# Optimization experiments

Hardware: AMD Instinct MI355X
Metric: run time of the kernel (lower is better)

## Reference

```python
import jax, jax.numpy as jnp
import numpy as np

N = 50000
F_IN = 128
HID0, HID1 = 64, 32
HEADS = 2
E = 800000
NEG_SLOPE = 0.2


def gat_conv(x, edge_index, W, att_src, att_dst, bias, heads, out_ch, concat):
    """PyG-style GATConv (add_self_loops=True, negative_slope=0.2, eval mode)."""
    n = x.shape[0]
    loop = jnp.arange(n, dtype=edge_index.dtype)
    src = jnp.concatenate([edge_index[0], loop])  # message sources (x_j)
    dst = jnp.concatenate([edge_index[1], loop])  # message targets (x_i)
    h = (x @ W).reshape(n, heads, out_ch)                # [N,H,C]
    a_src = jnp.einsum('nhc,hc->nh', h, att_src)          # [N,H]
    a_dst = jnp.einsum('nhc,hc->nh', h, att_dst)          # [N,H]
    e = jax.nn.leaky_relu(a_src[src] + a_dst[dst], NEG_SLOPE)  # [E+N,H]
    # segment softmax over incoming edges of each destination node
    m = jax.ops.segment_max(e, dst, num_segments=n)
    m = jnp.where(jnp.isfinite(m), m, 0.0)
    p = jnp.exp(e - m[dst])
    s = jax.ops.segment_sum(p, dst, num_segments=n)
    alpha = p / (s[dst] + 1e-16)                          # [E+N,H]
    msg = h[src] * alpha[:, :, None]                      # [E+N,H,C]
    out = jax.ops.segment_sum(msg, dst, num_segments=n)   # [N,H,C]
    out = out.reshape(n, heads * out_ch) if concat else out.mean(axis=1)
    return out + bias


def setup_inputs() -> dict:
    key = jax.random.key(0)
    ks = jax.random.split(key, 10)
    sc1 = 1.0 / np.sqrt(F_IN)
    sc2 = 1.0 / np.sqrt(HEADS * HID0)
    return {
        'x': jax.random.normal(ks[0], (N, F_IN), dtype=jnp.float32),
        'edge_index': jax.random.randint(ks[1], (2, E), 0, N, dtype=jnp.int64),
        'W1': jax.random.normal(ks[2], (F_IN, HEADS * HID0), dtype=jnp.float32) * sc1,
        'att_src1': jax.random.normal(ks[3], (HEADS, HID0), dtype=jnp.float32) * sc1,
        'att_dst1': jax.random.normal(ks[4], (HEADS, HID0), dtype=jnp.float32) * sc1,
        'bias1': jnp.zeros((HEADS * HID0,), dtype=jnp.float32),
        'W2': jax.random.normal(ks[5], (HEADS * HID0, HEADS * HID1), dtype=jnp.float32) * sc2,
        'att_src2': jax.random.normal(ks[6], (HEADS, HID1), dtype=jnp.float32) * sc2,
        'att_dst2': jax.random.normal(ks[7], (HEADS, HID1), dtype=jnp.float32) * sc2,
        'bias2': jnp.zeros((HID1,), dtype=jnp.float32),
    }


def reference(x, edge_index, W1, att_src1, att_dst1, bias1, W2, att_src2, att_dst2, bias2):
    h = gat_conv(x, edge_index, W1, att_src1, att_dst1, bias1, HEADS, HID0, concat=True)
    h = jax.nn.relu(h)  # Dropout(0.6) is identity in eval mode
    out = gat_conv(h, edge_index, W2, att_src2, att_dst2, bias2, HEADS, HID1, concat=False)
    return out
```

## Files before the change

### kernel.cpp

```cpp
#include <hip/hip_runtime.h>
#include <hip/hip_bf16.h>

#define NN 50000
#define FIN 128
#define NH 2
#define C1 64
#define C2 32
#define NE 800000
#define NEG 0.2f

typedef unsigned int uint32;

__device__ __forceinline__ float lrelu(float v) { return v > 0.0f ? v : NEG * v; }
__device__ __forceinline__ float dot4(float4 a, float4 b) {
    return a.x * b.x + a.y * b.y + a.z * b.z + a.w * b.w;
}
__device__ __forceinline__ uint32 packbf2(float a, float b) {
    uint32 ua = __float_as_uint(a), ub = __float_as_uint(b);
    ua += 0x7fffu + ((ua >> 16) & 1u);
    ub += 0x7fffu + ((ub >> 16) & 1u);
    return (ua >> 16) | (ub & 0xffff0000u);
}

__global__ void zero_ints(int* __restrict__ a, int n) {
    for (int i = blockIdx.x * blockDim.x + threadIdx.x; i < n;
         i += gridDim.x * blockDim.x) a[i] = 0;
}

__global__ void hist_dst(const int* __restrict__ ei, int* __restrict__ deg) {
    const int i = blockIdx.x * blockDim.x + threadIdx.x;
    if (i >= NE) return;
    atomicAdd(&deg[ei[NE + i]], 1);
}

__global__ void scan_blocks(const int* __restrict__ deg, int* __restrict__ offs,
                            int* __restrict__ bsum) {
    __shared__ int sm[256];
    const int t = threadIdx.x;
    const int i = blockIdx.x * 256 + t;
    const int v = (i < NN) ? deg[i] : 0;
    sm[t] = v;
    __syncthreads();
    int x = v;
    #pragma unroll
    for (int d = 1; d < 256; d <<= 1) {
        const int y = (t >= d) ? sm[t - d] : 0;
        __syncthreads();
        x += y; sm[t] = x;
        __syncthreads();
    }
    if (i < NN) offs[i] = x - v;
    if (t == 255) bsum[blockIdx.x] = x;
}

__global__ void scan_bsums(int* __restrict__ bsum, int nb) {
    __shared__ int sm[256];
    const int t = threadIdx.x;
    const int v = (t < nb) ? bsum[t] : 0;
    sm[t] = v;
    __syncthreads();
    int x = v;
    #pragma unroll
    for (int d = 1; d < 256; d <<= 1) {
        const int y = (t >= d) ? sm[t - d] : 0;
        __syncthreads();
        x += y; sm[t] = x;
        __syncthreads();
    }
    if (t < nb) bsum[t] = x - v;
}

__global__ void scan_add(int* __restrict__ offs, const int* __restrict__ bsum) {
    const int i = blockIdx.x * 256 + threadIdx.x;
    if (i < NN) offs[i] += bsum[blockIdx.x];
}

__global__ void csr_scatter(const int* __restrict__ ei, const int* __restrict__ offs,
                            int* __restrict__ fill, int* __restrict__ esrc) {
    const int i = blockIdx.x * blockDim.x + threadIdx.x;
    if (i >= NE) return;
    const int src = ei[i], dst = ei[NE + i];
    const int pos = offs[dst] + atomicAdd(&fill[dst], 1);
    esrc[pos] = src;
}

template<int BN, bool RELU_BIAS, bool WRITE_Y, bool WRITE_H16>
__global__ __launch_bounds__(256, 2) void gemm_k128(const float* __restrict__ X,
                                                    const float* __restrict__ Wm,
                                                    const float* __restrict__ bias,
                                                    const float* __restrict__ attS,
                                                    const float* __restrict__ attD,
                                                    float* __restrict__ Y,
                                                    uint32* __restrict__ H16,
                                                    float* __restrict__ asrcO,
                                                    float* __restrict__ adstO, int M) {
    constexpr int GROUPS = BN / 16;
    constexpr int BM = 256 / GROUPS;
    constexpr int CS = BN / 4;
    __shared__ __align__(16) float Xs[BM][33];
    __shared__ __align__(16) float Ws[32][BN];

    const int tid = threadIdx.x;
    const int r  = tid / GROUPS;
    const int g  = tid % GROUPS;
    const int rowBase = blockIdx.x * BM;

    float4 acc0 = {0,0,0,0}, acc1 = {0,0,0,0}, acc2 = {0,0,0,0}, acc3 = {0,0,0,0};

    for (int kk = 0; kk < 4; ++kk) {
        constexpr int XV = BM * 8;
        #pragma unroll
        for (int i = tid; i < XV; i += 256) {
            const int xr = i >> 3, xc = (i & 7) * 4;
            const int grow = rowBase + xr;
            float4 v = {0,0,0,0};
            if (grow < M) {
                v = *reinterpret_cast<const float4*>(&X[grow * FIN + kk * 32 + xc]);
                if (RELU_BIAS) {
                    const float4 b = *reinterpret_cast<const float4*>(&bias[kk * 32 + xc]);
                    v.x = fmaxf(v.x + b.x, 0.0f);
                    v.y = fmaxf(v.y + b.y, 0.0f);
                    v.z = fmaxf(v.z + b.z, 0.0f);
                    v.w = fmaxf(v.w + b.w, 0.0f);
                }
            }
            Xs[xr][xc] = v.x; Xs[xr][xc+1] = v.y; Xs[xr][xc+2] = v.z; Xs[xr][xc+3] = v.w;
        }
        constexpr int WV = 32 * BN / 4;
        #pragma unroll
        for (int i = tid; i < WV; i += 256) {
            const int wr = i / (BN / 4), wc = (i % (BN / 4)) * 4;
            *reinterpret_cast<float4*>(&Ws[wr][wc]) =
                *reinterpret_cast<const float4*>(&Wm[(kk * 32 + wr) * BN + wc]);
        }
        __syncthreads();
        #pragma unroll
        for (int k = 0; k < 32; ++k) {
            const float xv = Xs[r][k];
            const float4 w0 = *reinterpret_cast<const float4*>(&Ws[k][g * 4]);
            const float4 w1 = *reinterpret_cast<const float4*>(&Ws[k][g * 4 + CS]);
            const float4 w2 = *reinterpret_cast<const float4*>(&Ws[k][g * 4 + 2 * CS]);
            const float4 w3 = *reinterpret_cast<const float4*>(&Ws[k][g * 4 + 3 * CS]);
            acc0.x += xv * w0.x; acc0.y += xv * w0.y; acc0.z += xv * w0.z; acc0.w += xv * w0.w;
            acc1.x += xv * w1.x; acc1.y += xv * w1.y; acc1.z += xv * w1.z; acc1.w += xv * w1.w;
            acc2.x += xv * w2.x; acc2.y += xv * w2.y; acc2.z += xv * w2.z; acc2.w += xv * w2.w;
            acc3.x += xv * w3.x; acc3.y += xv * w3.y; acc3.z += xv * w3.z; acc3.w += xv * w3.w;
        }
        __syncthreads();
    }

    const int grow = rowBase + r;
    if (grow < M) {
        if (WRITE_Y) {
            float* yrow = &Y[grow * BN + g * 4];
            *reinterpret_cast<float4*>(yrow)          = acc0;
            *reinterpret_cast<float4*>(yrow + CS)     = acc1;
            *reinterpret_cast<float4*>(yrow + 2 * CS) = acc2;
            *reinterpret_cast<float4*>(yrow + 3 * CS) = acc3;
        }
        if (WRITE_H16) {
            uint32* hrow = &H16[grow * (BN / 2)];
            uint2 u;
            u.x = packbf2(acc0.x, acc0.y); u.y = packbf2(acc0.z, acc0.w);
            *reinterpret_cast<uint2*>(&hrow[g * 2])              = u;
            u.x = packbf2(acc1.x, acc1.y); u.y = packbf2(acc1.z, acc1.w);
            *reinterpret_cast<uint2*>(&hrow[g * 2 + CS / 2])     = u;
            u.x = packbf2(acc2.x, acc2.y); u.y = packbf2(acc2.z, acc2.w);
            *reinterpret_cast<uint2*>(&hrow[g * 2 + CS])         = u;
            u.x = packbf2(acc3.x, acc3.y); u.y = packbf2(acc3.z, acc3.w);
            *reinterpret_cast<uint2*>(&hrow[g * 2 + 3 * CS / 2]) = u;
        }
    }
    const float4* avs = reinterpret_cast<const float4*>(attS);
    const float4* avd = reinterpret_cast<const float4*>(attD);
    float ps0 = dot4(acc0, avs[g])              + dot4(acc1, avs[g + GROUPS]);
    float ps1 = dot4(acc2, avs[g + 2 * GROUPS]) + dot4(acc3, avs[g + 3 * GROUPS]);
    float pd0 = dot4(acc0, avd[g])              + dot4(acc1, avd[g + GROUPS]);
    float pd1 = dot4(acc2, avd[g + 2 * GROUPS]) + dot4(acc3, avd[g + 3 * GROUPS]);
    #pragma unroll
    for (int d = 1; d < GROUPS; d <<= 1) {
        ps0 += __shfl_xor(ps0, d);
        ps1 += __shfl_xor(ps1, d);
        pd0 += __shfl_xor(pd0, d);
        pd1 += __shfl_xor(pd1, d);
    }
    if (g == 0 && grow < M) {
        asrcO[grow * 2]     = ps0;
        asrcO[grow * 2 + 1] = ps1;
        adstO[grow * 2]     = pd0;
        adstO[grow * 2 + 1] = pd1;
    }
}

__global__ __launch_bounds__(256) void gat_dst1(const int* __restrict__ esrc,
                                                const int* __restrict__ offs,
                                                const uint32* __restrict__ H16,
                                                const float* __restrict__ asrc,
                                                const float* __restrict__ adst,
                                                float* __restrict__ out) {
    const int wid  = (blockIdx.x * blockDim.x + threadIdx.x) >> 6;
    const int lane = threadIdx.x & 63;
    if (wid >= NN) return;
    const int dst = wid;
    const int beg = offs[dst];
    const int end = (dst == NN - 1) ? NE : offs[dst + 1];
    const int deg = end - beg;
    const float2 ad = *reinterpret_cast<const float2*>(&adst[dst * 2]);

    int   s0  = 0;
    float pe0 = -INFINITY, pe1 = -INFINITY;
    float m0  = -INFINITY, m1  = -INFINITY;
    for (int j = lane; j < deg; j += 64) {
        const int s = esrc[beg + j];
        const float2 a = *reinterpret_cast<const float2*>(&asrc[s * 2]);
        const float f0 = lrelu(a.x + ad.x);
        const float f1 = lrelu(a.y + ad.y);
        if (j == lane) { s0 = s; pe0 = f0; pe1 = f1; }
        m0 = fmaxf(m0, f0); m1 = fmaxf(m1, f1);
    }
    const float2 aself = *reinterpret_cast<const float2*>(&asrc[dst * 2]);
    const float es0 = lrelu(aself.x + ad.x);
    const float es1 = lrelu(aself.y + ad.y);
    m0 = fmaxf(m0, es0); m1 = fmaxf(m1, es1);
    #pragma unroll
    for (int d = 1; d < 64; d <<= 1) {
        m0 = fmaxf(m0, __shfl_xor(m0, d));
        m1 = fmaxf(m1, __shfl_xor(m1, d));
    }
    const int h = lane >> 5;
    const float m = h ? m1 : m0;

    float l;
    float2 acc;
    {
        const float px = __expf((h ? es1 : es0) - m);
        l = px;
        const uint32 u = H16[dst * 64 + lane];
        acc.x = px * __uint_as_float(u << 16);
        acc.y = px * __uint_as_float(u & 0xffff0000u);
    }
    const int jmax = deg < 64 ? deg : 64;
    for (int j = 0; j < jmax; ++j) {
        const int s = __shfl(s0, j);
        const float t0 = __shfl(pe0, j), t1 = __shfl(pe1, j);
        const float p = __expf((h ? t1 : t0) - m);
        const uint32 u = H16[s * 64 + lane];
        l += p;
        acc.x += p * __uint_as_float(u << 16);
        acc.y += p * __uint_as_float(u & 0xffff0000u);
    }
    for (int j = 64; j < deg; ++j) {
        const int s = esrc[beg + j];
        const float2 a = *reinterpret_cast<const float2*>(&asrc[s * 2]);
        const float p = __expf(lrelu((h ? a.y : a.x) + (h ? ad.y : ad.x)) - m);
        const uint32 u = H16[s * 64 + lane];
        l += p;
        acc.x += p * __uint_as_float(u << 16);
        acc.y += p * __uint_as_float(u & 0xffff0000u);
    }
    const float inv = 1.0f / (l + 1e-16f);
    float2 res; res.x = acc.x * inv; res.y = acc.y * inv;
    *reinterpret_cast<float2*>(&out[dst * 128 + lane * 2]) = res;
}

__global__ __launch_bounds__(256) void gat_dst2(const int* __restrict__ esrc,
                                                const int* __restrict__ offs,
                                                const float* __restrict__ Hf,
                                                const float* __restrict__ asrc,
                                                const float* __restrict__ adst,
                                                const float* __restrict__ bias,
                                                float* __restrict__ out) {
    const int wid  = (blockIdx.x * blockDim.x + threadIdx.x) >> 6;
    const int lane = threadIdx.x & 63;
    if (wid >= NN) return;
    const int dst = wid;
    const int beg = offs[dst];
    const int end = (dst == NN - 1) ? NE : offs[dst + 1];
    const int deg = end - beg;
    const float2 ad = *reinterpret_cast<const float2*>(&adst[dst * 2]);

    int   s0  = 0;
    float pe0 = -INFINITY, pe1 = -INFINITY;
    float m0  = -INFINITY, m1  = -INFINITY;
    for (int j = lane; j < deg; j += 64) {
        const int s = esrc[beg + j];
        const float2 a = *reinterpret_cast<const float2*>(&asrc[s * 2]);
        const float f0 = lrelu(a.x + ad.x);
        const float f1 = lrelu(a.y + ad.y);
        if (j == lane) { s0 = s; pe0 = f0; pe1 = f1; }
        m0 = fmaxf(m0, f0); m1 = fmaxf(m1, f1);
    }
    const float2 aself = *reinterpret_cast<const float2*>(&asrc[dst * 2]);
    const float es0 = lrelu(aself.x + ad.x);
    const float es1 = lrelu(aself.y + ad.y);
    m0 = fmaxf(m0, es0); m1 = fmaxf(m1, es1);
    #pragma unroll
    for (int d = 1; d < 64; d <<= 1) {
        m0 = fmaxf(m0, __shfl_xor(m0, d));
        m1 = fmaxf(m1, __shfl_xor(m1, d));
    }
    const int h = lane >> 5;
    const float m = h ? m1 : m0;

    float l, acc;
    {
        const float px = __expf((h ? es1 : es0) - m);
        l = px;
        acc = px * Hf[dst * 64 + lane];
    }
    const int jmax = deg < 64 ? deg : 64;
    for (int j = 0; j < jmax; ++j) {
        const int s = __shfl(s0, j);
        const float t0 = __shfl(pe0, j), t1 = __shfl(pe1, j);
        const float p = __expf((h ? t1 : t0) - m);
        const float hv = Hf[s * 64 + lane];
        l += p;
        acc += p * hv;
    }
    for (int j = 64; j < deg; ++j) {
        const int s = esrc[beg + j];
        const float2 a = *reinterpret_cast<const float2*>(&asrc[s * 2]);
        const float p = __expf(lrelu((h ? a.y : a.x) + (h ? ad.y : ad.x)) - m);
        l += p;
        acc += p * Hf[s * 64 + lane];
    }
    float r = acc / (l + 1e-16f);
    r += __shfl_xor(r, 32);
    if (lane < 32) out[dst * 32 + lane] = 0.5f * r + bias[lane];
}

extern "C" void kernel_launch(void* const* d_in, const int* in_sizes, int n_in,
                              void* d_out, int out_size, void* d_ws, size_t ws_size,
                              hipStream_t stream) {
    const float* x   = (const float*)d_in[0];
    const int*   ei  = (const int*)d_in[1];
    const float* W1  = (const float*)d_in[2];
    const float* as1 = (const float*)d_in[3];
    const float* ad1 = (const float*)d_in[4];
    const float* b1  = (const float*)d_in[5];
    const float* W2  = (const float*)d_in[6];
    const float* as2 = (const float*)d_in[7];
    const float* ad2 = (const float*)d_in[8];
    const float* b2  = (const float*)d_in[9];
    float* out = (float*)d_out;

    float* ws = (float*)d_ws;
    size_t off = 0;
    float* out1  = ws + off; off += (size_t)NN * FIN;
    float* h2f   = ws + off; off += (size_t)NN * C1;
    float* asrc1 = ws + off; off += (size_t)NN * NH;
    float* adst1 = ws + off; off += (size_t)NN * NH;
    float* asrc2 = ws + off; off += (size_t)NN * NH;
    float* adst2 = ws + off; off += (size_t)NN * NH;
    uint32* h16  = (uint32*)(ws + off); off += (size_t)NN * 64;
    int* ibase = (int*)(ws + off);
    int* deg   = ibase;
    int* fill  = ibase + NN;
    int* offs  = ibase + 2 * NN;
    int* bsum  = ibase + 3 * NN;
    int* esrc  = ibase + 3 * NN + 256;

    const int B = 256;
    constexpr int NB_SCAN = (NN + 255) / 256;

    zero_ints<<<128, B, 0, stream>>>(deg, 2 * NN);
    hist_dst<<<(NE + B - 1) / B, B, 0, stream>>>(ei, deg);
    scan_blocks<<<NB_SCAN, 256, 0, stream>>>(deg, offs, bsum);
    scan_bsums<<<1, 256, 0, stream>>>(bsum, NB_SCAN);
    scan_add<<<NB_SCAN, 256, 0, stream>>>(offs, bsum);
    csr_scatter<<<(NE + B - 1) / B, B, 0, stream>>>(ei, offs, fill, esrc);

    gemm_k128<128, false, false, true><<<(NN + 31) / 32, B, 0, stream>>>(
        x, W1, nullptr, as1, ad1, nullptr, h16, asrc1, adst1, NN);
    gat_dst1<<<(NN * 64 + B - 1) / B, B, 0, stream>>>(
        esrc, offs, h16, asrc1, adst1, out1);

    gemm_k128<64, true, true, false><<<(NN + 63) / 64, B, 0, stream>>>(
        out1, W2, b1, as2, ad2, h2f, nullptr, asrc2, adst2, NN);
    gat_dst2<<<(NN * 64 + B - 1) / B, B, 0, stream>>>(
        esrc, offs, h2f, asrc2, adst2, b2, out);
}
```

Before: 383.4 us.

## Double-buffer GEMM tiles via direct global-to-LDS loads, two rows per thread

The feature GEMM now stages X and W tiles straight into LDS with the global_load_lds builtin, double-buffered so the next K-chunk loads while the current one is computed. It uses an XOR-swizzled X layout and gives each thread two rows, which doubles the tile height and halves the grid. The layer-1 bias+ReLU moves from the second GEMM's load path into gat_dst1's epilogue. The cost is more accumulator registers and LDS per block, and reliance on the ordering and layout rules of direct-to-LDS loads.

New measurement: 366.5 us. -4.4%, faster.

```diff
diff --git a/kernel.cpp b/kernel.cpp
--- a/kernel.cpp
+++ b/kernel.cpp
@@ -20,6 +20,11 @@
     ua += 0x7fffu + ((ua >> 16) & 1u);
     ub += 0x7fffu + ((ub >> 16) & 1u);
     return (ua >> 16) | (ub & 0xffff0000u);
+}
+__device__ __forceinline__ void gload16(const float* g, float* l) {
+    __builtin_amdgcn_global_load_lds(
+        (const __attribute__((address_space(1))) unsigned int*)g,
+        (__attribute__((address_space(3))) unsigned int*)l, 16, 0, 0);
 }
 
 __global__ void zero_ints(int* __restrict__ a, int n) {
@@ -84,10 +89,9 @@
     esrc[pos] = src;
 }
 
-template<int BN, bool RELU_BIAS, bool WRITE_Y, bool WRITE_H16>
+template<int BN, bool WRITE_Y, bool WRITE_H16>
 __global__ __launch_bounds__(256, 2) void gemm_k128(const float* __restrict__ X,
                                                     const float* __restrict__ Wm,
-                                                    const float* __restrict__ bias,
                                                     const float* __restrict__ attS,
                                                     const float* __restrict__ attD,
                                                     float* __restrict__ Y,
@@ -95,100 +99,125 @@
                                                     float* __restrict__ asrcO,
                                                     float* __restrict__ adstO, int M) {
     constexpr int GROUPS = BN / 16;
-    constexpr int BM = 256 / GROUPS;
+    constexpr int NR = 256 / GROUPS;
+    constexpr int BM = NR * 2;
     constexpr int CS = BN / 4;
-    __shared__ __align__(16) float Xs[BM][33];
-    __shared__ __align__(16) float Ws[32][BN];
+    constexpr int NXC = BM / 32;
+    constexpr int NWC = BN / 32;
+    __shared__ __align__(16) float Xs[2][BM * 32];
+    __shared__ __align__(16) float Ws[2][32 * BN];
 
     const int tid = threadIdx.x;
     const int r  = tid / GROUPS;
     const int g  = tid % GROUPS;
+    const int g4 = g * 4;
+    const int wv = tid >> 6;
     const int rowBase = blockIdx.x * BM;
-
-    float4 acc0 = {0,0,0,0}, acc1 = {0,0,0,0}, acc2 = {0,0,0,0}, acc3 = {0,0,0,0};
-
+    const int rr = r & 7;
+
+    auto stage = [&](int kk, int b) {
+        float* XsB = &Xs[b][0];
+        float* WsB = &Ws[b][0];
+        #pragma unroll
+        for (int t = 0; t < NXC; ++t) {
+            const int d  = t * 256 + tid;
+            const int xr = d >> 3;
+            const int kc = (d & 7) ^ (xr & 7);
+            int xrow = rowBase + xr;
+            if (xrow >= M) xrow = M - 1;
+            gload16(X + xrow * 128 + kk * 32 + kc * 4,
+                    XsB + (t * 256 + wv * 64) * 4);
+        }
+        #pragma unroll
+        for (int t = 0; t < NWC; ++t) {
+            const int d = t * 256 + tid;
+            gload16(Wm + kk * 32 * BN + d * 4,
+                    WsB + (t * 256 + wv * 64) * 4);
+        }
+    };
+
+    float4 aA[4], aB[4];
+    #pragma unroll
+    for (int j = 0; j < 4; ++j) { aA[j] = {0,0,0,0}; aB[j] = {0,0,0,0}; }
+
+    stage(0, 0);
+    __syncthreads();
     for (int kk = 0; kk < 4; ++kk) {
-        constexpr int XV = BM * 8;
+        const int cur = kk & 1;
+        if (kk < 3) stage(kk + 1, cur ^ 1);
+        const float* XsC = &Xs[cur][0];
+        const float* WsC = &Ws[cur][0];
+        auto step = [&](int k, float xv0, float xv1) {
+            const float* wp = WsC + k * BN + g4;
+            const float4 w0 = *reinterpret_cast<const float4*>(wp);
+            const float4 w1 = *reinterpret_cast<const float4*>(wp + CS);
+            const float4 w2 = *reinterpret_cast<const float4*>(wp + 2 * CS);
+            const float4 w3 = *reinterpret_cast<const float4*>(wp + 3 * CS);
+            aA[0].x += xv0*w0.x; aA[0].y += xv0*w0.y; aA[0].z += xv0*w0.z; aA[0].w += xv0*w0.w;
+            aA[1].x += xv0*w1.x; aA[1].y += xv0*w1.y; aA[1].z += xv0*w1.z; aA[1].w += xv0*w1.w;
+            aA[2].x += xv0*w2.x; aA[2].y += xv0*w2.y; aA[2].z += xv0*w2.z; aA[2].w += xv0*w2.w;
+            aA[3].x += xv0*w3.x; aA[3].y += xv0*w3.y; aA[3].z += xv0*w3.z; aA[3].w += xv0*w3.w;
+            aB[0].x += xv1*w0.x; aB[0].y += xv1*w0.y; aB[0].z += xv1*w0.z; aB[0].w += xv1*w0.w;
+            aB[1].x += xv1*w1.x; aB[1].y += xv1*w1.y; aB[1].z += xv1*w1.z; aB[1].w += xv1*w1.w;
+            aB[2].x += xv1*w2.x; aB[2].y += xv1*w2.y; aB[2].z += xv1*w2.z; aB[2].w += xv1*w2.w;
+            aB[3].x += xv1*w3.x; aB[3].y += xv1*w3.y; aB[3].z += xv1*w3.z; aB[3].w += xv1*w3.w;
+        };
         #pragma unroll
-        for (int i = tid; i < XV; i += 256) {
-            const int xr = i >> 3, xc = (i & 7) * 4;
-            const int grow = rowBase + xr;
-            float4 v = {0,0,0,0};
-            if (grow < M) {
-                v = *reinterpret_cast<const float4*>(&X[grow * FIN + kk * 32 + xc]);
-                if (RELU_BIAS) {
-                    const float4 b = *reinterpret_cast<const float4*>(&bias[kk * 32 + xc]);
-                    v.x = fmaxf(v.x + b.x, 0.0f);
-                    v.y = fmaxf(v.y + b.y, 0.0f);
-                    v.z = fmaxf(v.z + b.z, 0.0f);
-                    v.w = fmaxf(v.w + b.w, 0.0f);
+        for (int kc = 0; kc < 8; ++kc) {
+            const float4 xq0 = *reinterpret_cast<const float4*>(
+                XsC + (r * 8 + (kc ^ rr)) * 4);
+            const float4 xq1 = *reinterpret_cast<const float4*>(
+                XsC + ((r + NR) * 8 + (kc ^ rr)) * 4);
+            step(kc * 4 + 0, xq0.x, xq1.x);
+            step(kc * 4 + 1, xq0.y, xq1.y);
+            step(kc * 4 + 2, xq0.z, xq1.z);
+            step(kc * 4 + 3, xq0.w, xq1.w);
+        }
+        __syncthreads();
+    }
+
+    const float4* avs = reinterpret_cast<const float4*>(attS);
+    const float4* avd = reinterpret_cast<const float4*>(attD);
+    #pragma unroll
+    for (int p = 0; p < 2; ++p) {
+        const float4* a = p ? aB : aA;
+        const int grow = rowBase + r + NR * p;
+        if (grow < M) {
+            if (WRITE_Y) {
+                float* yrow = &Y[grow * BN + g4];
+                *reinterpret_cast<float4*>(yrow)          = a[0];
+                *reinterpret_cast<float4*>(yrow + CS)     = a[1];
+                *reinterpret_cast<float4*>(yrow + 2 * CS) = a[2];
+                *reinterpret_cast<float4*>(yrow + 3 * CS) = a[3];
+            }
+            if (WRITE_H16) {
+                uint32* hrow = &H16[grow * (BN / 2)];
+                #pragma unroll
+                for (int j = 0; j < 4; ++j) {
+                    uint2 u;
+                    u.x = packbf2(a[j].x, a[j].y);
+                    u.y = packbf2(a[j].z, a[j].w);
+                    *reinterpret_cast<uint2*>(&hrow[g * 2 + j * (CS / 2)]) = u;
                 }
             }
-            Xs[xr][xc] = v.x; Xs[xr][xc+1] = v.y; Xs[xr][xc+2] = v.z; Xs[xr][xc+3] = v.w;
-        }
-        constexpr int WV = 32 * BN / 4;
+        }
+        float ps0 = dot4(a[0], avs[g])              + dot4(a[1], avs[g + GROUPS]);
+        float ps1 = dot4(a[2], avs[g + 2 * GROUPS]) + dot4(a[3], avs[g + 3 * GROUPS]);
+        float pd0 = dot4(a[0], avd[g])              + dot4(a[1], avd[g + GROUPS]);
+        float pd1 = dot4(a[2], avd[g + 2 * GROUPS]) + dot4(a[3], avd[g + 3 * GROUPS]);
         #pragma unroll
-        for (int i = tid; i < WV; i += 256) {
-            const int wr = i / (BN / 4), wc = (i % (BN / 4)) * 4;
-            *reinterpret_cast<float4*>(&Ws[wr][wc]) =
-                *reinterpret_cast<const float4*>(&Wm[(kk * 32 + wr) * BN + wc]);
-        }
-        __syncthreads();
-        #pragma unroll
-        for (int k = 0; k < 32; ++k) {
-            const float xv = Xs[r][k];
-            const float4 w0 = *reinterpret_cast<const float4*>(&Ws[k][g * 4]);
-            const float4 w1 = *reinterpret_cast<const float4*>(&Ws[k][g * 4 + CS]);
-            const float4 w2 = *reinterpret_cast<const float4*>(&Ws[k][g * 4 + 2 * CS]);
-            const float4 w3 = *reinterpret_cast<const float4*>(&Ws[k][g * 4 + 3 * CS]);
-            acc0.x += xv * w0.x; acc0.y += xv * w0.y; acc0.z += xv * w0.z; acc0.w += xv * w0.w;
-            acc1.x += xv * w1.x; acc1.y += xv * w1.y; acc1.z += xv * w1.z; acc1.w += xv * w1.w;
-            acc2.x += xv * w2.x; acc2.y += xv * w2.y; acc2.z += xv * w2.z; acc2.w += xv * w2.w;
-            acc3.x += xv * w3.x; acc3.y += xv * w3.y; acc3.z += xv * w3.z; acc3.w += xv * w3.w;
-        }
-        __syncthreads();
-    }
-
-    const int grow = rowBase + r;
-    if (grow < M) {
-        if (WRITE_Y) {
-            float* yrow = &Y[grow * BN + g * 4];
-            *reinterpret_cast<float4*>(yrow)          = acc0;
-            *reinterpret_cast<float4*>(yrow + CS)     = acc1;
-            *reinterpret_cast<float4*>(yrow + 2 * CS) = acc2;
-            *reinterpret_cast<float4*>(yrow + 3 * CS) = acc3;
-        }
-        if (WRITE_H16) {
-            uint32* hrow = &H16[grow * (BN / 2)];
-            uint2 u;
-            u.x = packbf2(acc0.x, acc0.y); u.y = packbf2(acc0.z, acc0.w);
-            *reinterpret_cast<uint2*>(&hrow[g * 2])              = u;
-            u.x = packbf2(acc1.x, acc1.y); u.y = packbf2(acc1.z, acc1.w);
-            *reinterpret_cast<uint2*>(&hrow[g * 2 + CS / 2])     = u;
-            u.x = packbf2(acc2.x, acc2.y); u.y = packbf2(acc2.z, acc2.w);
-            *reinterpret_cast<uint2*>(&hrow[g * 2 + CS])         = u;
-            u.x = packbf2(acc3.x, acc3.y); u.y = packbf2(acc3.z, acc3.w);
-            *reinterpret_cast<uint2*>(&hrow[g * 2 + 3 * CS / 2]) = u;
-        }
-    }
-    const float4* avs = reinterpret_cast<const float4*>(attS);
-    const float4* avd = reinterpret_cast<const float4*>(attD);
-    float ps0 = dot4(acc0, avs[g])              + dot4(acc1, avs[g + GROUPS]);
-    float ps1 = dot4(acc2, avs[g + 2 * GROUPS]) + dot4(acc3, avs[g + 3 * GROUPS]);
-    float pd0 = dot4(acc0, avd[g])              + dot4(acc1, avd[g + GROUPS]);
-    float pd1 = dot4(acc2, avd[g + 2 * GROUPS]) + dot4(acc3, avd[g + 3 * GROUPS]);
-    #pragma unroll
-    for (int d = 1; d < GROUPS; d <<= 1) {
-        ps0 += __shfl_xor(ps0, d);
-        ps1 += __shfl_xor(ps1, d);
-        pd0 += __shfl_xor(pd0, d);
-        pd1 += __shfl_xor(pd1, d);
-    }
-    if (g == 0 && grow < M) {
-        asrcO[grow * 2]     = ps0;
-        asrcO[grow * 2 + 1] = ps1;
-        adstO[grow * 2]     = pd0;
-        adstO[grow * 2 + 1] = pd1;
+        for (int d = 1; d < GROUPS; d <<= 1) {
+            ps0 += __shfl_xor(ps0, d);
+            ps1 += __shfl_xor(ps1, d);
+            pd0 += __shfl_xor(pd0, d);
+            pd1 += __shfl_xor(pd1, d);
+        }
+        if (g == 0 && grow < M) {
+            asrcO[grow * 2]     = ps0;
+            asrcO[grow * 2 + 1] = ps1;
+            adstO[grow * 2]     = pd0;
+            adstO[grow * 2 + 1] = pd1;
+        }
     }
 }
 
@@ -197,6 +226,7 @@
                                                 const uint32* __restrict__ H16,
                                                 const float* __restrict__ asrc,
                                                 const float* __restrict__ adst,
+                                                const float* __restrict__ bias1,
                                                 float* __restrict__ out) {
     const int wid  = (blockIdx.x * blockDim.x + threadIdx.x) >> 6;
     const int lane = threadIdx.x & 63;
@@ -259,7 +289,10 @@
         acc.y += p * __uint_as_float(u & 0xffff0000u);
     }
     const float inv = 1.0f / (l + 1e-16f);
-    float2 res; res.x = acc.x * inv; res.y = acc.y * inv;
+    const float2 bb = *reinterpret_cast<const float2*>(&bias1[lane * 2]);
+    float2 res;
+    res.x = fmaxf(acc.x * inv + bb.x, 0.0f);
+    res.y = fmaxf(acc.y * inv + bb.y, 0.0f);
     *reinterpret_cast<float2*>(&out[dst * 128 + lane * 2]) = res;
 }
 
@@ -370,13 +403,13 @@
     scan_add<<<NB_SCAN, 256, 0, stream>>>(offs, bsum);
     csr_scatter<<<(NE + B - 1) / B, B, 0, stream>>>(ei, offs, fill, esrc);
 
-    gemm_k128<128, false, false, true><<<(NN + 31) / 32, B, 0, stream>>>(
-        x, W1, nullptr, as1, ad1, nullptr, h16, asrc1, adst1, NN);
+    gemm_k128<128, false, true><<<(NN + 63) / 64, B, 0, stream>>>(
+        x, W1, as1, ad1, nullptr, h16, asrc1, adst1, NN);
     gat_dst1<<<(NN * 64 + B - 1) / B, B, 0, stream>>>(
-        esrc, offs, h16, asrc1, adst1, out1);
-
-    gemm_k128<64, true, true, false><<<(NN + 63) / 64, B, 0, stream>>>(
-        out1, W2, b1, as2, ad2, h2f, nullptr, asrc2, adst2, NN);
+        esrc, offs, h16, asrc1, adst1, b1, out1);
+
+    gemm_k128<64, true, false><<<(NN + 127) / 128, B, 0, stream>>>(
+        out1, W2, as2, ad2, h2f, nullptr, asrc2, adst2, NN);
     gat_dst2<<<(NN * 64 + B - 1) / B, B, 0, stream>>>(
         esrc, offs, h2f, asrc2, adst2, b2, out);
 }
```
